# Performance work log

Measured on AMD Instinct MI355X. Metric: run time of the kernel, lower is better.

Reference implementation:

```python
import jax, jax.numpy as jnp
import numpy as np

DIM = 1024
HEADS = 16
HDIM = DIM // HEADS
MLP_HID = 4096
LN_EPS = 1e-5
NORM_EPS = 1e-12  # F.normalize eps


def _layernorm(x, g, b):
    mu = jnp.mean(x, axis=-1, keepdims=True)
    var = jnp.mean(jnp.square(x - mu), axis=-1, keepdims=True)
    return (x - mu) / jnp.sqrt(var + LN_EPS) * g + b


def _l2norm(x):
    n = jnp.linalg.norm(x, axis=-1, keepdims=True)
    return x / jnp.maximum(n, NORM_EPS)


def setup_inputs() -> dict:
    key = jax.random.key(0)
    ks = jax.random.split(key, 8)
    s = 0.02
    x = jax.random.normal(ks[0], (2, 2048, DIM), dtype=jnp.float32)
    w_qkv = jax.random.normal(ks[1], (3 * DIM, DIM), dtype=jnp.float32) * s  # torch Linear weight (out,in)
    w_proj = jax.random.normal(ks[2], (DIM, DIM), dtype=jnp.float32) * s
    temp = jnp.ones((HEADS, 1, 1), dtype=jnp.float32)
    w1 = jax.random.normal(ks[3], (MLP_HID, DIM), dtype=jnp.float32) * s
    b1 = jnp.zeros((MLP_HID,), dtype=jnp.float32)
    w2 = jax.random.normal(ks[4], (DIM, MLP_HID), dtype=jnp.float32) * s
    b2 = jnp.zeros((DIM,), dtype=jnp.float32)
    ln1_g = jnp.ones((DIM,), dtype=jnp.float32)
    ln1_b = jnp.zeros((DIM,), dtype=jnp.float32)
    ln2_g = jnp.ones((DIM,), dtype=jnp.float32)
    ln2_b = jnp.zeros((DIM,), dtype=jnp.float32)
    return {"x": x, "ln1_g": ln1_g, "ln1_b": ln1_b, "w_qkv": w_qkv,
            "w_proj": w_proj, "temp": temp, "ln2_g": ln2_g, "ln2_b": ln2_b,
            "w1": w1, "b1": b1, "w2": w2, "b2": b2}


def reference(x, ln1_g, ln1_b, w_qkv, w_proj, temp, ln2_g, ln2_b, w1, b1, w2, b2):
    b, n, c = x.shape
    # --- MHSA with L2-normalized q,k and learnable per-head temperature ---
    h = _layernorm(x, ln1_g, ln1_b)
    qkv = h @ w_qkv.T                             # [b,n,3c]
    qkv = qkv.reshape(b, n, 3, HEADS, HDIM).transpose(2, 0, 3, 1, 4)  # [3,b,h,n,d]
    q, k, v = qkv[0], qkv[1], qkv[2]
    q = _l2norm(q)
    k = _l2norm(k)
    attn = jnp.einsum('bhnd,bhmd->bhnm', q, k) * temp  # temp [h,1,1] broadcasts
    attn = jax.nn.softmax(attn, axis=-1)
    out = jnp.einsum('bhnm,bhmd->bhnd', attn, v)       # [b,h,n,d]
    out = out.transpose(0, 2, 1, 3).reshape(b, n, c)
    x = x + out @ w_proj.T
    # --- MLP ---
    h = _layernorm(x, ln2_g, ln2_b)
    h = jax.nn.gelu(h @ w1.T + b1, approximate=False)
    x = x + h @ w2.T + b2
    return x
```

## Files before the change

### kernel.cpp

```cpp
#include <hip/hip_runtime.h>
#include <cstdint>
#include <cstddef>

typedef unsigned short u16;
typedef __attribute__((ext_vector_type(8))) short short8;
typedef __attribute__((ext_vector_type(4))) float f32x4;
typedef __attribute__((ext_vector_type(4))) float float4v;
typedef __attribute__((ext_vector_type(4))) u16 u16x4;

__device__ __forceinline__ u16 f2bf(float f) {
  union { float f; uint32_t u; } v; v.f = f;
  uint32_t u = v.u;
  return (u16)((u + 0x7FFFu + ((u >> 16) & 1u)) >> 16);
}
__device__ __forceinline__ float bf2f(u16 s) {
  union { uint32_t u; float f; } v; v.u = ((uint32_t)s) << 16; return v.f;
}

__device__ __forceinline__ float fast_exp2(float x) {
#if __has_builtin(__builtin_amdgcn_exp2f)
  return __builtin_amdgcn_exp2f(x);
#else
  return exp2f(x);
#endif
}

__device__ __forceinline__ void gload16(const u16* g, u16* l) {
  __builtin_amdgcn_global_load_lds((const __attribute__((address_space(1))) void*)g,
                                   (__attribute__((address_space(3))) void*)l,
                                   16, 0, 0);
}

__global__ __launch_bounds__(256) void k_cvt(const float* __restrict__ in, u16* __restrict__ out, int n4) {
  int i = blockIdx.x * 256 + threadIdx.x;
  if (i >= n4) return;
  float4v v = *(const float4v*)(in + (size_t)i * 4);
  u16x4 o;
  #pragma unroll
  for (int j = 0; j < 4; j++) o[j] = f2bf(v[j]);
  *(u16x4*)(out + (size_t)i * 4) = o;
}

__global__ __launch_bounds__(256) void k_ln(const float* __restrict__ x, const float* __restrict__ g,
                                            const float* __restrict__ b, u16* __restrict__ out) {
  int row = blockIdx.x, tid = threadIdx.x;
  int wid = tid >> 6;
  const float* xr = x + (size_t)row * 1024;
  float4v v = *(const float4v*)(xr + tid * 4);
  float s = v[0] + v[1] + v[2] + v[3];
  float sq = v[0]*v[0] + v[1]*v[1] + v[2]*v[2] + v[3]*v[3];
  #pragma unroll
  for (int m = 1; m <= 32; m <<= 1) { s += __shfl_xor(s, m); sq += __shfl_xor(sq, m); }
  __shared__ float ss[4], ssq[4];
  if ((tid & 63) == 0) { ss[wid] = s; ssq[wid] = sq; }
  __syncthreads();
  s = ss[0] + ss[1] + ss[2] + ss[3];
  sq = ssq[0] + ssq[1] + ssq[2] + ssq[3];
  float mu = s * (1.0f/1024.0f);
  float var = sq * (1.0f/1024.0f) - mu*mu;
  float rs = rsqrtf(var + 1e-5f);
  u16x4 o;
  #pragma unroll
  for (int j = 0; j < 4; j++) {
    float y = (v[j] - mu) * rs * g[tid*4+j] + b[tid*4+j];
    o[j] = f2bf(y);
  }
  *(u16x4*)(out + (size_t)row * 1024 + tid * 4) = o;
}

template<int EPI>
__global__ __launch_bounds__(256) void k_gemm(const u16* __restrict__ A, const u16* __restrict__ B,
                                              const float* __restrict__ bias, u16* __restrict__ Cb,
                                              int M, int N, int K, int Ksub) {
  __shared__ __align__(16) u16 As[128*64];
  __shared__ __align__(16) u16 Bs[128*64];
  int tid = threadIdx.x;
  int gx = gridDim.x;
  int lin = blockIdx.y * gx + blockIdx.x;
  int nwg = gx * gridDim.y;
  int cpx = nwg >> 3;
  int swz = (lin & 7) * cpx + (lin >> 3);
  int bx = swz % gx, by = swz / gx;
  int m0 = by * 128, n0 = bx * 128;
  int kbase = blockIdx.z * Ksub;
  int wid = tid >> 6, lane = tid & 63;
  int wr = wid >> 1, wc = wid & 1;
  int l15 = lane & 15, l16 = lane >> 4;
  int gslot = (tid & 7) ^ ((tid >> 3) & 7);
  int srow = tid >> 3;

  f32x4 acc[4][4] = {};
  int nt = Ksub >> 6;

  for (int t = 0; t < nt; ++t) {
    int kb = kbase + (t << 6);
    #pragma unroll
    for (int i = 0; i < 4; i++) {
      int row = i*32 + srow;
      gload16(A + (size_t)(m0+row)*K + kb + gslot*8, &As[i*2048 + wid*512]);
      gload16(B + (size_t)(n0+row)*K + kb + gslot*8, &Bs[i*2048 + wid*512]);
    }
    __syncthreads();
    #pragma unroll
    for (int ks = 0; ks < 2; ks++) {
      short8 af[4], bfr[4];
      #pragma unroll
      for (int m = 0; m < 4; m++) {
        int row = wr*64 + m*16 + l15;
        af[m] = *(const short8*)&As[row*64 + (((ks*4 + l16) ^ (row & 7)) * 8)];
      }
      #pragma unroll
      for (int n = 0; n < 4; n++) {
        int row = wc*64 + n*16 + l15;
        bfr[n] = *(const short8*)&Bs[row*64 + (((ks*4 + l16) ^ (row & 7)) * 8)];
      }
      #pragma unroll
      for (int m = 0; m < 4; m++)
        #pragma unroll
        for (int n = 0; n < 4; n++)
          acc[m][n] = __builtin_amdgcn_mfma_f32_16x16x32_bf16(af[m], bfr[n], acc[m][n], 0, 0, 0);
    }
    __syncthreads();
  }

  size_t zoff = (EPI == 6) ? (size_t)blockIdx.z * M * N : 0;
  #pragma unroll
  for (int m = 0; m < 4; m++) {
    #pragma unroll
    for (int n = 0; n < 4; n++) {
      int col = n0 + wc*64 + n*16 + l15;
      #pragma unroll
      for (int r = 0; r < 4; r++) {
        int row = m0 + wr*64 + m*16 + l16*4 + r;
        float v = acc[m][n][r];
        if constexpr (EPI == 2) { v += bias[col]; v = 0.5f*v*(1.0f + erff(v*0.70710678118f)); }
        Cb[zoff + (size_t)row*N + col] = f2bf(v);
      }
    }
  }
}

__global__ __launch_bounds__(256) void k_red2(const float* __restrict__ x, const u16* __restrict__ P,
                                              float* __restrict__ x1) {
  int i = blockIdx.x * 256 + threadIdx.x;
  float4v v = *(const float4v*)(x + (size_t)i * 4);
  #pragma unroll
  for (int z = 0; z < 2; z++) {
    u16x4 p = *(const u16x4*)(P + (size_t)z * 4194304 + (size_t)i * 4);
    #pragma unroll
    for (int j = 0; j < 4; j++) v[j] += bf2f(p[j]);
  }
  *(float4v*)(x1 + (size_t)i * 4) = v;
}

__global__ __launch_bounds__(256) void k_red4(const float* __restrict__ x1, const float* __restrict__ b2,
                                              const u16* __restrict__ Q, float* __restrict__ out) {
  int i = blockIdx.x * 256 + threadIdx.x;
  float4v v = *(const float4v*)(x1 + (size_t)i * 4);
  float4v bb = *(const float4v*)(b2 + (size_t)(i & 255) * 4);
  #pragma unroll
  for (int j = 0; j < 4; j++) v[j] += bb[j];
  #pragma unroll
  for (int z = 0; z < 4; z++) {
    u16x4 p = *(const u16x4*)(Q + (size_t)z * 4194304 + (size_t)i * 4);
    #pragma unroll
    for (int j = 0; j < 4; j++) v[j] += bf2f(p[j]);
  }
  *(float4v*)(out + (size_t)i * 4) = v;
}

__global__ __launch_bounds__(256) void k_prep(const u16* __restrict__ qkv, const float* __restrict__ temp,
                                              u16* __restrict__ Qn, u16* __restrict__ Kn, u16* __restrict__ Vt) {
  int grp = blockIdx.x, bh = blockIdx.y;
  int b = bh >> 4, h = bh & 15;
  int tid = threadIdx.x, wid = tid >> 6, lane = tid & 63;
  int n0 = grp * 64;
  __shared__ __align__(16) u16 vs[64*64];
  float tmp = temp[h] * 1.44269504f;
  for (int j = 0; j < 16; j++) {
    int tl = wid + 4*j;
    size_t roff = (size_t)((b*2048) + n0 + tl) * 3072;
    float q = bf2f(qkv[roff + h*64 + lane]);
    float k = bf2f(qkv[roff + 1024 + h*64 + lane]);
    u16 vraw = qkv[roff + 2048 + h*64 + lane];
    float sq = q*q, sk = k*k;
    #pragma unroll
    for (int m = 1; m <= 32; m <<= 1) { sq += __shfl_xor(sq, m); sk += __shfl_xor(sk, m); }
    float qs = tmp / fmaxf(sqrtf(sq), 1e-12f);
    float ksc = 1.0f / fmaxf(sqrtf(sk), 1e-12f);
    size_t obase = ((size_t)bh*2048 + n0 + tl)*64 + lane;
    Qn[obase] = f2bf(q * qs);
    Kn[obase] = f2bf(k * ksc);
    vs[tl*64 + lane] = vraw;
  }
  __syncthreads();
  int d = tid & 63, chunk = tid >> 6;
  u16 vals[16];
  #pragma unroll
  for (int jj = 0; jj < 16; jj++) vals[jj] = vs[(chunk*16 + jj)*64 + d];
  short8 w0, w1v;
  #pragma unroll
  for (int j = 0; j < 8; j++) { w0[j] = (short)vals[j]; w1v[j] = (short)vals[8+j]; }
  size_t vo = ((size_t)bh*64 + d)*2048 + n0 + chunk*16;
  *(short8*)(Vt + vo) = w0;
  *(short8*)(Vt + vo + 8) = w1v;
}

__global__ __launch_bounds__(256) void k_attn(const u16* __restrict__ Qn, const u16* __restrict__ Kn,
                                              const u16* __restrict__ Vt, const float* __restrict__ temp,
                                              u16* __restrict__ Out) {
  __shared__ __align__(16) u16 Ks[2][64*64];
  __shared__ __align__(16) u16 Vs[2][64*64];
  __shared__ __align__(16) u16 Ps[4*16*64];
  int qg = blockIdx.x, bh = blockIdx.y;
  int b = bh >> 4, h = bh & 15;
  int tid = threadIdx.x, wid = tid >> 6, lane = tid & 63;
  int l15 = lane & 15, l16 = lane >> 4;
  size_t base = (size_t)bh * 2048 * 64;
  size_t vbase = (size_t)bh * 64 * 2048;
  int q0 = qg*64 + wid*16;
  float m2 = fabsf(temp[h]) * 1.44269504f;
  short8 qf[2];
  #pragma unroll
  for (int ks = 0; ks < 2; ks++)
    qf[ks] = *(const short8*)(Qn + base + (size_t)(q0 + l15)*64 + ks*32 + l16*8);
  f32x4 o[4] = {};
  float lrow = 0.f;
  u16* Pw = Ps + wid*16*64;
  uint32_t* Pw32 = (uint32_t*)Pw;

  auto STAGE = [&](int bsel, int kv0) {
    #pragma unroll
    for (int i = 0; i < 2; i++) {
      int base_row = wid*16 + i*8;
      int row = base_row + (lane >> 3);
      int gslot = (lane & 7) ^ (row & 7);
      gload16(Kn + base + (size_t)(kv0 + row)*64 + gslot*8, &Ks[bsel][base_row*64]);
      gload16(Vt + vbase + (size_t)row*2048 + kv0 + gslot*8, &Vs[bsel][base_row*64]);
    }
  };

  STAGE(0, 0);
  __syncthreads();
  int cur = 0;
  for (int kv0 = 0; kv0 < 2048; kv0 += 64) {
    if (kv0 + 64 < 2048) STAGE(cur ^ 1, kv0 + 64);
    f32x4 s[4] = {};
    #pragma unroll
    for (int ks = 0; ks < 2; ks++) {
      short8 kf[4];
      #pragma unroll
      for (int nt = 0; nt < 4; nt++) {
        int row = nt*16 + l15;
        kf[nt] = *(const short8*)&Ks[cur][row*64 + (((ks*4 + l16) ^ (row&7))*8)];
      }
      #pragma unroll
      for (int nt = 0; nt < 4; nt++)
        s[nt] = __builtin_amdgcn_mfma_f32_16x16x32_bf16(kf[nt], qf[ks], s[nt], 0, 0, 0);
    }
    float tsum = 0.f;
    #pragma unroll
    for (int nt = 0; nt < 4; nt++) {
      #pragma unroll
      for (int rp = 0; rp < 2; rp++) {
        float p0 = fast_exp2(s[nt][2*rp]   - m2);
        float p1 = fast_exp2(s[nt][2*rp+1] - m2);
        tsum += p0 + p1;
        uint32_t pk;
        asm("v_cvt_pk_bf16_f32 %0, %1, %2" : "=v"(pk) : "v"(p0), "v"(p1));
        int w = nt*8 + l16*2 + rp;
        int slot = w >> 2;
        Pw32[l15*32 + ((slot ^ (l15 & 7))*4) + (w & 3)] = pk;
      }
    }
    lrow += tsum;
    asm volatile("s_waitcnt lgkmcnt(0)" ::: "memory");
    __builtin_amdgcn_sched_barrier(0);
    #pragma unroll
    for (int ks = 0; ks < 2; ks++) {
      short8 pf = *(const short8*)&Pw[l15*64 + (((ks*4 + l16) ^ (l15&7))*8)];
      short8 vf[4];
      #pragma unroll
      for (int dt = 0; dt < 4; dt++) {
        int row = dt*16 + l15;
        vf[dt] = *(const short8*)&Vs[cur][row*64 + (((ks*4 + l16) ^ (row&7))*8)];
      }
      #pragma unroll
      for (int dt = 0; dt < 4; dt++)
        o[dt] = __builtin_amdgcn_mfma_f32_16x16x32_bf16(vf[dt], pf, o[dt], 0, 0, 0);
    }
    __syncthreads();
    cur ^= 1;
  }
  lrow += __shfl_xor(lrow, 16);
  lrow += __shfl_xor(lrow, 32);
  float rl = 1.0f / lrow;
  int tok = b*2048 + q0 + l15;
  #pragma unroll
  for (int dt = 0; dt < 4; dt++) {
    u16x4 ov;
    #pragma unroll
    for (int r = 0; r < 4; r++) ov[r] = f2bf(o[dt][r] * rl);
    *(u16x4*)(Out + (size_t)tok*1024 + h*64 + dt*16 + l16*4) = ov;
  }
}

static constexpr size_t OFF_WQKV  = 0;
static constexpr size_t OFF_WPROJ = OFF_WQKV  + 6291456;
static constexpr size_t OFF_W1    = OFF_WPROJ + 2097152;
static constexpr size_t OFF_W2    = OFF_W1    + 8388608;
static constexpr size_t OFF_HBF   = OFF_W2    + 8388608;
static constexpr size_t OFF_H2BF  = OFF_HBF   + 8388608;
static constexpr size_t OFF_QKVBF = OFF_H2BF  + 8388608;
static constexpr size_t OFF_QN    = OFF_QKVBF + 25165824;
static constexpr size_t OFF_KN    = OFF_QN    + 8388608;
static constexpr size_t OFF_VT    = OFF_KN    + 8388608;
static constexpr size_t OFF_AOUT  = OFF_VT    + 8388608;
static constexpr size_t OFF_X1    = OFF_AOUT  + 8388608;
static constexpr size_t OFF_HID   = OFF_X1    + 16777216;
static constexpr size_t OFF_P     = OFF_QN;

extern "C" void kernel_launch(void* const* d_in, const int* in_sizes, int n_in,
                              void* d_out, int out_size, void* d_ws, size_t ws_size,
                              hipStream_t stream) {
  (void)in_sizes; (void)n_in; (void)out_size; (void)ws_size;
  const float* x     = (const float*)d_in[0];
  const float* ln1g  = (const float*)d_in[1];
  const float* ln1b  = (const float*)d_in[2];
  const float* wqkv  = (const float*)d_in[3];
  const float* wproj = (const float*)d_in[4];
  const float* temp  = (const float*)d_in[5];
  const float* ln2g  = (const float*)d_in[6];
  const float* ln2b  = (const float*)d_in[7];
  const float* w1    = (const float*)d_in[8];
  const float* b1    = (const float*)d_in[9];
  const float* w2    = (const float*)d_in[10];
  const float* b2    = (const float*)d_in[11];

  char* ws = (char*)d_ws;
  u16* wqkv_bf  = (u16*)(ws + OFF_WQKV);
  u16* wproj_bf = (u16*)(ws + OFF_WPROJ);
  u16* w1_bf    = (u16*)(ws + OFF_W1);
  u16* w2_bf    = (u16*)(ws + OFF_W2);
  u16* h_bf     = (u16*)(ws + OFF_HBF);
  u16* h2_bf    = (u16*)(ws + OFF_H2BF);
  u16* qkv_bf   = (u16*)(ws + OFF_QKVBF);
  u16* Qn       = (u16*)(ws + OFF_QN);
  u16* Kn       = (u16*)(ws + OFF_KN);
  u16* Vt       = (u16*)(ws + OFF_VT);
  u16* aout_bf  = (u16*)(ws + OFF_AOUT);
  float* x1     = (float*)(ws + OFF_X1);
  u16* hid_bf   = (u16*)(ws + OFF_HID);
  u16* part     = (u16*)(ws + OFF_P);
  float* outf   = (float*)d_out;

  k_cvt<<<3072, 256, 0, stream>>>(wqkv,  wqkv_bf,  786432);
  k_cvt<<<1024, 256, 0, stream>>>(wproj, wproj_bf, 262144);
  k_cvt<<<4096, 256, 0, stream>>>(w1,    w1_bf,    1048576);
  k_cvt<<<4096, 256, 0, stream>>>(w2,    w2_bf,    1048576);

  k_ln<<<4096, 256, 0, stream>>>(x, ln1g, ln1b, h_bf);
  k_gemm<4><<<dim3(24, 32), 256, 0, stream>>>(h_bf, wqkv_bf, nullptr, qkv_bf, 4096, 3072, 1024, 1024);
  k_prep<<<dim3(32, 32), 256, 0, stream>>>(qkv_bf, temp, Qn, Kn, Vt);
  k_attn<<<dim3(32, 32), 256, 0, stream>>>(Qn, Kn, Vt, temp, aout_bf);
  k_gemm<6><<<dim3(8, 32, 2), 256, 0, stream>>>(aout_bf, wproj_bf, nullptr, part, 4096, 1024, 1024, 512);
  k_red2<<<4096, 256, 0, stream>>>(x, part, x1);
  k_ln<<<4096, 256, 0, stream>>>(x1, ln2g, ln2b, h2_bf);
  k_gemm<2><<<dim3(32, 32), 256, 0, stream>>>(h2_bf, w1_bf, b1, hid_bf, 4096, 4096, 1024, 1024);
  k_gemm<6><<<dim3(8, 32, 4), 256, 0, stream>>>(hid_bf, w2_bf, nullptr, part, 4096, 1024, 4096, 1024);
  k_red4<<<4096, 256, 0, stream>>>(x1, b2, part, outf);
}
```

Baseline: 285.1 us.

## Replace 128x128 GEMM with 256x256 triple-buffered 512-thread GEMM

Replaces the 128x128-tile, 256-thread GEMM with a 256x256-tile, 512-thread kernel. It uses a three-stage dynamic-shared-memory pipeline with explicit vmcnt waits and a single barrier per K=32 step, and raises MFMA priority around the compute block. The projection GEMM now uses 4-way split-K written into the hidden buffer, and the two reduction kernels are merged into one templated kernel. The goal is more data reuse per tile and less barrier and load stall time. The cost is fewer workgroups (192 for QKV), which risks underfilling the CUs, plus heavier register pressure.

Result: faster. 268.5 us (-5.8%).

```diff
diff --git a/kernel.cpp b/kernel.cpp
--- a/kernel.cpp
+++ b/kernel.cpp
@@ -69,11 +69,10 @@
 }
 
 template<int EPI>
-__global__ __launch_bounds__(256) void k_gemm(const u16* __restrict__ A, const u16* __restrict__ B,
-                                              const float* __restrict__ bias, u16* __restrict__ Cb,
-                                              int M, int N, int K, int Ksub) {
-  __shared__ __align__(16) u16 As[128*64];
-  __shared__ __align__(16) u16 Bs[128*64];
+__global__ __launch_bounds__(512, 2) void k_g256(const u16* __restrict__ A, const u16* __restrict__ B,
+                                                 const float* __restrict__ bias, u16* __restrict__ Cb,
+                                                 int M, int N, int K, int Ksub) {
+  extern __shared__ __align__(16) u16 smem[];
   int tid = threadIdx.x;
   int gx = gridDim.x;
   int lin = blockIdx.y * gx + blockIdx.x;
@@ -81,58 +80,78 @@
   int cpx = nwg >> 3;
   int swz = (lin & 7) * cpx + (lin >> 3);
   int bx = swz % gx, by = swz / gx;
-  int m0 = by * 128, n0 = bx * 128;
+  int m0 = by * 256, n0 = bx * 256;
   int kbase = blockIdx.z * Ksub;
   int wid = tid >> 6, lane = tid & 63;
-  int wr = wid >> 1, wc = wid & 1;
+  int wm = wid >> 2, wn = wid & 3;
   int l15 = lane & 15, l16 = lane >> 4;
-  int gslot = (tid & 7) ^ ((tid >> 3) & 7);
-  int srow = tid >> 3;
-
-  f32x4 acc[4][4] = {};
-  int nt = Ksub >> 6;
+
+  f32x4 acc[8][4] = {};
+  int nt = Ksub >> 5;
+
+  auto STAGE = [&](int bsel, int kb) {
+    u16* abase = smem + bsel * 16384;
+    u16* bbase = abase + 8192;
+    #pragma unroll
+    for (int i = 0; i < 2; i++) {
+      int c = i*512 + tid;
+      int R = c >> 3, p = c & 7;
+      int sp = p ^ (R & 7);
+      int r = 2*R + (sp >> 2);
+      int g = sp & 3;
+      gload16(A + (size_t)(m0 + r)*K + kb + g*8, abase + c*8);
+      gload16(B + (size_t)(n0 + r)*K + kb + g*8, bbase + c*8);
+    }
+  };
+
+  STAGE(0, kbase);
+  STAGE(1, kbase + 32);
 
   for (int t = 0; t < nt; ++t) {
-    int kb = kbase + (t << 6);
-    #pragma unroll
-    for (int i = 0; i < 4; i++) {
-      int row = i*32 + srow;
-      gload16(A + (size_t)(m0+row)*K + kb + gslot*8, &As[i*2048 + wid*512]);
-      gload16(B + (size_t)(n0+row)*K + kb + gslot*8, &Bs[i*2048 + wid*512]);
-    }
-    __syncthreads();
-    #pragma unroll
-    for (int ks = 0; ks < 2; ks++) {
-      short8 af[4], bfr[4];
-      #pragma unroll
-      for (int m = 0; m < 4; m++) {
-        int row = wr*64 + m*16 + l15;
-        af[m] = *(const short8*)&As[row*64 + (((ks*4 + l16) ^ (row & 7)) * 8)];
-      }
-      #pragma unroll
-      for (int n = 0; n < 4; n++) {
-        int row = wc*64 + n*16 + l15;
-        bfr[n] = *(const short8*)&Bs[row*64 + (((ks*4 + l16) ^ (row & 7)) * 8)];
-      }
-      #pragma unroll
-      for (int m = 0; m < 4; m++)
-        #pragma unroll
-        for (int n = 0; n < 4; n++)
-          acc[m][n] = __builtin_amdgcn_mfma_f32_16x16x32_bf16(af[m], bfr[n], acc[m][n], 0, 0, 0);
-    }
-    __syncthreads();
+    if (t + 1 < nt) asm volatile("s_waitcnt vmcnt(4)" ::: "memory");
+    else            asm volatile("s_waitcnt vmcnt(0)" ::: "memory");
+    __builtin_amdgcn_sched_barrier(0);
+    __builtin_amdgcn_s_barrier();
+    __builtin_amdgcn_sched_barrier(0);
+    if (t + 2 < nt) STAGE((t + 2) % 3, kbase + (t + 2) * 32);
+    const u16* ab = smem + (t % 3) * 16384;
+    const u16* bb = ab + 8192;
+    short8 af[8], bf[4];
+    #pragma unroll
+    for (int mf = 0; mf < 8; mf++) {
+      int r = wm*128 + mf*16 + l15;
+      int R = r >> 1;
+      int sp = ((r & 1)*4 + l16) ^ (R & 7);
+      af[mf] = *(const short8*)(ab + R*64 + sp*8);
+    }
+    #pragma unroll
+    for (int nf = 0; nf < 4; nf++) {
+      int r = wn*64 + nf*16 + l15;
+      int R = r >> 1;
+      int sp = ((r & 1)*4 + l16) ^ (R & 7);
+      bf[nf] = *(const short8*)(bb + R*64 + sp*8);
+    }
+    asm volatile("s_waitcnt lgkmcnt(0)" ::: "memory");
+    __builtin_amdgcn_sched_barrier(0);
+    __builtin_amdgcn_s_setprio(1);
+    #pragma unroll
+    for (int mf = 0; mf < 8; mf++)
+      #pragma unroll
+      for (int nf = 0; nf < 4; nf++)
+        acc[mf][nf] = __builtin_amdgcn_mfma_f32_16x16x32_bf16(af[mf], bf[nf], acc[mf][nf], 0, 0, 0);
+    __builtin_amdgcn_s_setprio(0);
   }
 
   size_t zoff = (EPI == 6) ? (size_t)blockIdx.z * M * N : 0;
   #pragma unroll
-  for (int m = 0; m < 4; m++) {
-    #pragma unroll
-    for (int n = 0; n < 4; n++) {
-      int col = n0 + wc*64 + n*16 + l15;
+  for (int mf = 0; mf < 8; mf++) {
+    #pragma unroll
+    for (int nf = 0; nf < 4; nf++) {
+      int col = n0 + wn*64 + nf*16 + l15;
       #pragma unroll
       for (int r = 0; r < 4; r++) {
-        int row = m0 + wr*64 + m*16 + l16*4 + r;
-        float v = acc[m][n][r];
+        int row = m0 + wm*128 + mf*16 + l16*4 + r;
+        float v = acc[mf][nf][r];
         if constexpr (EPI == 2) { v += bias[col]; v = 0.5f*v*(1.0f + erff(v*0.70710678118f)); }
         Cb[zoff + (size_t)row*N + col] = f2bf(v);
       }
@@ -140,29 +159,19 @@
   }
 }
 
-__global__ __launch_bounds__(256) void k_red2(const float* __restrict__ x, const u16* __restrict__ P,
-                                              float* __restrict__ x1) {
+template<int HASB>
+__global__ __launch_bounds__(256) void k_red4(const float* __restrict__ base, const float* __restrict__ bias,
+                                              const u16* __restrict__ P, float* __restrict__ out) {
   int i = blockIdx.x * 256 + threadIdx.x;
-  float4v v = *(const float4v*)(x + (size_t)i * 4);
-  #pragma unroll
-  for (int z = 0; z < 2; z++) {
+  float4v v = *(const float4v*)(base + (size_t)i * 4);
+  if constexpr (HASB) {
+    float4v bb = *(const float4v*)(bias + (size_t)(i & 255) * 4);
+    #pragma unroll
+    for (int j = 0; j < 4; j++) v[j] += bb[j];
+  }
+  #pragma unroll
+  for (int z = 0; z < 4; z++) {
     u16x4 p = *(const u16x4*)(P + (size_t)z * 4194304 + (size_t)i * 4);
-    #pragma unroll
-    for (int j = 0; j < 4; j++) v[j] += bf2f(p[j]);
-  }
-  *(float4v*)(x1 + (size_t)i * 4) = v;
-}
-
-__global__ __launch_bounds__(256) void k_red4(const float* __restrict__ x1, const float* __restrict__ b2,
-                                              const u16* __restrict__ Q, float* __restrict__ out) {
-  int i = blockIdx.x * 256 + threadIdx.x;
-  float4v v = *(const float4v*)(x1 + (size_t)i * 4);
-  float4v bb = *(const float4v*)(b2 + (size_t)(i & 255) * 4);
-  #pragma unroll
-  for (int j = 0; j < 4; j++) v[j] += bb[j];
-  #pragma unroll
-  for (int z = 0; z < 4; z++) {
-    u16x4 p = *(const u16x4*)(Q + (size_t)z * 4194304 + (size_t)i * 4);
     #pragma unroll
     for (int j = 0; j < 4; j++) v[j] += bf2f(p[j]);
   }
@@ -318,7 +327,6 @@
 static constexpr size_t OFF_AOUT  = OFF_VT    + 8388608;
 static constexpr size_t OFF_X1    = OFF_AOUT  + 8388608;
 static constexpr size_t OFF_HID   = OFF_X1    + 16777216;
-static constexpr size_t OFF_P     = OFF_QN;
 
 extern "C" void kernel_launch(void* const* d_in, const int* in_sizes, int n_in,
                               void* d_out, int out_size, void* d_ws, size_t ws_size,
@@ -351,8 +359,17 @@
   u16* aout_bf  = (u16*)(ws + OFF_AOUT);
   float* x1     = (float*)(ws + OFF_X1);
   u16* hid_bf   = (u16*)(ws + OFF_HID);
-  u16* part     = (u16*)(ws + OFF_P);
+  u16* part_p   = (u16*)(ws + OFF_HID);
+  u16* part_m   = (u16*)(ws + OFF_QN);
   float* outf   = (float*)d_out;
+
+  static bool attr_done = false;
+  if (!attr_done) {
+    hipFuncSetAttribute((const void*)k_g256<2>, hipFuncAttributeMaxDynamicSharedMemorySize, 98304);
+    hipFuncSetAttribute((const void*)k_g256<4>, hipFuncAttributeMaxDynamicSharedMemorySize, 98304);
+    hipFuncSetAttribute((const void*)k_g256<6>, hipFuncAttributeMaxDynamicSharedMemorySize, 98304);
+    attr_done = true;
+  }
 
   k_cvt<<<3072, 256, 0, stream>>>(wqkv,  wqkv_bf,  786432);
   k_cvt<<<1024, 256, 0, stream>>>(wproj, wproj_bf, 262144);
@@ -360,13 +377,13 @@
   k_cvt<<<4096, 256, 0, stream>>>(w2,    w2_bf,    1048576);
 
   k_ln<<<4096, 256, 0, stream>>>(x, ln1g, ln1b, h_bf);
-  k_gemm<4><<<dim3(24, 32), 256, 0, stream>>>(h_bf, wqkv_bf, nullptr, qkv_bf, 4096, 3072, 1024, 1024);
+  k_g256<4><<<dim3(12, 16), 512, 98304, stream>>>(h_bf, wqkv_bf, nullptr, qkv_bf, 4096, 3072, 1024, 1024);
   k_prep<<<dim3(32, 32), 256, 0, stream>>>(qkv_bf, temp, Qn, Kn, Vt);
   k_attn<<<dim3(32, 32), 256, 0, stream>>>(Qn, Kn, Vt, temp, aout_bf);
-  k_gemm<6><<<dim3(8, 32, 2), 256, 0, stream>>>(aout_bf, wproj_bf, nullptr, part, 4096, 1024, 1024, 512);
-  k_red2<<<4096, 256, 0, stream>>>(x, part, x1);
+  k_g256<6><<<dim3(4, 16, 4), 512, 98304, stream>>>(aout_bf, wproj_bf, nullptr, part_p, 4096, 1024, 1024, 256);
+  k_red4<0><<<4096, 256, 0, stream>>>(x, nullptr, part_p, x1);
   k_ln<<<4096, 256, 0, stream>>>(x1, ln2g, ln2b, h2_bf);
-  k_gemm<2><<<dim3(32, 32), 256, 0, stream>>>(h2_bf, w1_bf, b1, hid_bf, 4096, 4096, 1024, 1024);
-  k_gemm<6><<<dim3(8, 32, 4), 256, 0, stream>>>(hid_bf, w2_bf, nullptr, part, 4096, 1024, 4096, 1024);
-  k_red4<<<4096, 256, 0, stream>>>(x1, b2, part, outf);
-}
+  k_g256<2><<<dim3(16, 16), 512, 98304, stream>>>(h2_bf, w1_bf, b1, hid_bf, 4096, 4096, 1024, 1024);
+  k_g256<6><<<dim3(4, 16, 4), 512, 98304, stream>>>(hid_bf, w2_bf, nullptr, part_m, 4096, 1024, 4096, 1024);
+  k_red4<1><<<4096, 256, 0, stream>>>(x1, b2, part_m, outf);
+}
```
